# Performance work log

Measured on AMD Instinct MI355X. Metric: run time of the kernel, lower is better.

## Reference

```python
import jax, jax.numpy as jnp
import numpy as np

N_NODES = 50000
N_EDGES = 600000
IN_F = 128
OUT_F = 128
SMALL = max(IN_F // 10, 1)  # floor(128/10) = 12
D_K = np.sqrt(SMALL).astype(np.float32)


def setup_inputs() -> dict:
    key = jax.random.key(0)
    ks = jax.random.split(key, 10)
    node_data = jax.random.normal(ks[0], (N_NODES, IN_F), dtype=jnp.float32)
    src = jax.random.randint(ks[1], (N_EDGES,), 0, N_NODES, dtype=jnp.int32)
    dst = jax.random.randint(ks[2], (N_EDGES,), 0, N_NODES, dtype=jnp.int32)
    s_q = 1.0 / np.sqrt(IN_F)
    Wq = jax.random.uniform(ks[3], (SMALL, IN_F), jnp.float32, -s_q, s_q)
    bq = jax.random.uniform(ks[4], (SMALL,), jnp.float32, -s_q, s_q)
    Wk = jax.random.uniform(ks[5], (SMALL, IN_F), jnp.float32, -s_q, s_q)
    bk = jax.random.uniform(ks[6], (SMALL,), jnp.float32, -s_q, s_q)
    W1 = jax.random.uniform(ks[7], (OUT_F, IN_F), jnp.float32, -s_q, s_q)
    W2 = jax.random.uniform(ks[8], (OUT_F, IN_F), jnp.float32, -s_q, s_q)
    b2 = jax.random.uniform(ks[9], (OUT_F,), jnp.float32, -s_q, s_q)
    return {"node_data": node_data, "src": src, "dst": dst,
            "Wq": Wq, "bq": bq, "Wk": Wk, "bk": bk,
            "W1": W1, "W2": W2, "b2": b2}


def reference(node_data, src, dst, Wq, bq, Wk, bk, W1, W2, b2):
    N = node_data.shape[0]
    # dgl.add_self_loop: append (i, i) for every node -> each dst has >= 1 edge
    loops = jnp.arange(N, dtype=src.dtype)
    s = jnp.concatenate([src, loops])
    d = jnp.concatenate([dst, loops])

    # query = Tanh(Linear), key = Linear  (shapes [N, SMALL])
    q = jnp.tanh(node_data @ Wq.T + bq)
    k = node_data @ Wk.T + bk

    # per-edge score: sum(query[src] * key[dst]) / sqrt(small)
    scores = jnp.sum(q[s] * k[d], axis=1) / D_K  # [E]

    # softmax over incoming edges of each dst node (segment softmax)
    seg_max = jax.ops.segment_max(scores, d, num_segments=N)
    w = jnp.exp(scores - seg_max[d])
    seg_sum = jax.ops.segment_sum(w, d, num_segments=N)
    w = w / seg_sum[d]  # [E]

    # weighted scatter-aggregate of src node inputs -> [N, IN_F]
    att = jax.ops.segment_sum(w[:, None] * node_data[s], d, num_segments=N)

    # DeepSetLayer: layer1(node_data) + layer2(node attention)
    x = node_data @ W1.T + (att @ W2.T + b2)
    # per-row L2 ('fro' over dim=1) normalization, then ReLU
    x = x / jnp.linalg.norm(x, axis=1, keepdims=True)
    return jax.nn.relu(x)
```

## Files before the change

### kernel.cpp

```cpp
#include <hip/hip_runtime.h>
#include <hip/hip_bf16.h>
#include <math.h>
#include <stdint.h>


#define IN_F 128
#define SMALL 12
#define QK_PAD 16
#define SCAN_ITEMS 8
#define SCAN_CHUNK 2048

typedef __attribute__((ext_vector_type(8))) _Float16 half8;
typedef __attribute__((ext_vector_type(8))) unsigned short ushort8;
typedef __attribute__((ext_vector_type(4))) float f32x4;

__device__ __forceinline__ float dot12(const float* __restrict__ qrow,
                                       float4 c0, float4 c1, float4 c2) {
    float4 a = ((const float4*)qrow)[0];
    float4 b = ((const float4*)qrow)[1];
    float4 c = ((const float4*)qrow)[2];
    return a.x*c0.x + a.y*c0.y + a.z*c0.z + a.w*c0.w
         + b.x*c1.x + b.y*c1.y + b.z*c1.z + b.w*c1.w
         + c.x*c2.x + c.y*c2.y + c.z*c2.z + c.w*c2.w;
}

__device__ __forceinline__ half8 ld_h8(const float* p) {
    float4 x0 = *(const float4*)p;
    float4 x1 = *(const float4*)(p + 4);
    half8 a;
    a[0] = (_Float16)x0.x; a[1] = (_Float16)x0.y;
    a[2] = (_Float16)x0.z; a[3] = (_Float16)x0.w;
    a[4] = (_Float16)x1.x; a[5] = (_Float16)x1.y;
    a[6] = (_Float16)x1.z; a[7] = (_Float16)x1.w;
    return a;
}

__global__ __launch_bounds__(256) void prep_kernel(
    const float* __restrict__ nd,
    const float* __restrict__ Wq, const float* __restrict__ bq,
    const float* __restrict__ Wk, const float* __restrict__ bk,
    const int* __restrict__ dst,
    const float* __restrict__ W1, const float* __restrict__ W2,
    float* __restrict__ q, float* __restrict__ kf,
    unsigned short* __restrict__ ndb, int* __restrict__ cnt,
    unsigned short* __restrict__ rank, unsigned short* __restrict__ Wc,
    int N, int E, int NBQK, int NBCNT)
{
    int t = threadIdx.x;
    int b = blockIdx.x;

    if (b < NBQK) {
        int wv = t >> 6;
        int lane = t & 63;
        int col = lane & 15;
        int quad = lane >> 4;
        int tbase = b * 64 + wv * 16;

        int arow = tbase + col;
        int rowc = (arow < N) ? arow : (N - 1);
        const float* ap = nd + (size_t)rowc * IN_F + quad * 8;
        unsigned short* np = ndb + (size_t)arow * IN_F + quad * 8;

        const float* w0 = ((col < 12) ? (Wq + (size_t)col * IN_F)
                                      : (Wk + (size_t)(col - 12) * IN_F)) + quad * 8;
        const float* w1 = Wk + (size_t)((col < 8) ? (col + 4) : 4) * IN_F + quad * 8;
        bool hasw1 = (col < 8);

        half8 zero = {};
        f32x4 acc0 = (f32x4)0.f, acc1 = (f32x4)0.f;
#pragma unroll
        for (int ks = 0; ks < 4; ks++) {
            int k0 = ks * 32;
            half8 a = ld_h8(ap + k0);
            if (arow < N) *(half8*)(np + k0) = a;
            half8 bb0 = ld_h8(w0 + k0);
            half8 bb1 = hasw1 ? ld_h8(w1 + k0) : zero;
            acc0 = __builtin_amdgcn_mfma_f32_16x16x32_f16(a, bb0, acc0, 0, 0, 0);
            acc1 = __builtin_amdgcn_mfma_f32_16x16x32_f16(a, bb1, acc1, 0, 0, 0);
        }
        float bias0 = (col < 12) ? bq[col] : bk[col - 12];
        float bias1 = (col < 8) ? bk[col + 4] : 0.f;
#pragma unroll
        for (int r = 0; r < 4; r++) {
            int node = tbase + quad * 4 + r;
            if (node < N) {
                float v0 = acc0[r] + bias0;
                if (col < 12) q[(size_t)node * QK_PAD + col] = tanhf(v0);
                else          kf[(size_t)node * QK_PAD + (col - 12)] = v0;
                if (hasw1)    kf[(size_t)node * QK_PAD + col + 4] = acc1[r] + bias1;
            }
        }
    } else if (b < NBQK + NBCNT) {
        int ET = E + N;
        int stride = NBCNT * 256;
        for (int i = (b - NBQK) * 256 + t; i < ET; i += stride) {
            int d = (i < E) ? dst[i] : (i - E);
            rank[i] = (unsigned short)atomicAdd(&cnt[d], 1);
        }
    } else {
        int idx = (b - NBQK - NBCNT) * 256 + t;
        int f = idx >> 8, k = idx & 255;
        float v = (k < 128) ? W1[f * 128 + k] : W2[f * 128 + (k - 128)];
        ((_Float16*)Wc)[idx] = (_Float16)v;
    }
}

__global__ __launch_bounds__(256) void scan_local_kernel(
    const int* __restrict__ cnt, int* __restrict__ off,
    int* __restrict__ bsum, int N)
{
    __shared__ int tsum[256];
    int t = threadIdx.x;
    int base = blockIdx.x * SCAN_CHUNK + t * SCAN_ITEMS;
    int v[SCAN_ITEMS];
    int s = 0;
#pragma unroll
    for (int i = 0; i < SCAN_ITEMS; i++) {
        int idx = base + i;
        v[i] = (idx < N) ? ((cnt[idx] + 7) & ~7) : 0;
        s += v[i];
    }
    tsum[t] = s;
    __syncthreads();
    for (int d = 1; d < 256; d <<= 1) {
        int x = (t >= d) ? tsum[t - d] : 0;
        __syncthreads();
        tsum[t] += x;
        __syncthreads();
    }
    int excl = (t == 0) ? 0 : tsum[t - 1];
#pragma unroll
    for (int i = 0; i < SCAN_ITEMS; i++) {
        int idx = base + i;
        if (idx < N) off[idx] = excl;
        excl += v[i];
    }
    if (t == 255) bsum[blockIdx.x] = tsum[255];
}

__global__ __launch_bounds__(256) void scan_add_kernel(
    int* __restrict__ off, const int* __restrict__ bsum, int N, int NB)
{
    __shared__ int pre2[2];
    int t = threadIdx.x;
    if (t == 0) {
        int p = 0, tot = 0;
        for (int i = 0; i < NB; i++) {
            int v = bsum[i];
            if (i < (int)blockIdx.x) p += v;
            tot += v;
        }
        pre2[0] = p; pre2[1] = tot;
    }
    __syncthreads();
    int add = pre2[0];
    if (blockIdx.x == 0 && t == 0) off[N] = pre2[1];

    int base = blockIdx.x * SCAN_CHUNK + t * SCAN_ITEMS;
#pragma unroll
    for (int i = 0; i < SCAN_ITEMS; i++) {
        int j = base + i;
        if (j < N) off[j] += add;
    }
}

__global__ __launch_bounds__(256) void scatter_kernel(
    const int* __restrict__ src, const int* __restrict__ dst,
    const int* __restrict__ off, const unsigned short* __restrict__ rank,
    unsigned short* __restrict__ esrc, int E, int N)
{
    int i = blockIdx.x * 256 + threadIdx.x;
    if (i >= E + N) return;
    int d, s;
    if (i < E) { d = dst[i]; s = src[i]; }
    else       { d = i - E; s = d; }
    esrc[off[d] + (int)rank[i]] = (unsigned short)s;
}

__global__ __launch_bounds__(256) void attn_kernel(
    const unsigned short* __restrict__ ndb, const float* __restrict__ q,
    const float* __restrict__ kf, const int* __restrict__ off,
    const int* __restrict__ cnt, const unsigned short* __restrict__ esrc,
    void* __restrict__ attv, int att16, int N)
{
    const float INVDK = 0.28867513459481287f;
    int t = threadIdx.x;
    int lane = t & 63;
    int l16 = lane & 15;
    int gbase = lane & 48;
    int wid = blockIdx.x * 16 + (t >> 4);
    if (wid >= N) return;

    int start = off[wid];
    int deg = cnt[wid];

    const float4* kp = (const float4*)(kf + (size_t)wid * QK_PAD);
    float4 c0 = kp[0], c1 = kp[1], c2 = kp[2];

    float acc[8];
#pragma unroll
    for (int j = 0; j < 8; j++) acc[j] = 0.f;
    float inv;

    const unsigned short* nb = ndb + l16 * 8;

#define ACCUM(hv, ww) do {                                                    \
        acc[0] += (ww) * (float)(hv)[0]; acc[1] += (ww) * (float)(hv)[1];     \
        acc[2] += (ww) * (float)(hv)[2]; acc[3] += (ww) * (float)(hv)[3];     \
        acc[4] += (ww) * (float)(hv)[4]; acc[5] += (ww) * (float)(hv)[5];     \
        acc[6] += (ww) * (float)(hv)[6]; acc[7] += (ww) * (float)(hv)[7];     \
    } while (0)

#define LOAD8(pfx, id)                                                        \
    half8 pfx##0 = *(const half8*)(nb + (size_t)(id)[0] * IN_F);              \
    half8 pfx##1 = *(const half8*)(nb + (size_t)(id)[1] * IN_F);              \
    half8 pfx##2 = *(const half8*)(nb + (size_t)(id)[2] * IN_F);              \
    half8 pfx##3 = *(const half8*)(nb + (size_t)(id)[3] * IN_F);              \
    half8 pfx##4 = *(const half8*)(nb + (size_t)(id)[4] * IN_F);              \
    half8 pfx##5 = *(const half8*)(nb + (size_t)(id)[5] * IN_F);              \
    half8 pfx##6 = *(const half8*)(nb + (size_t)(id)[6] * IN_F);              \
    half8 pfx##7 = *(const half8*)(nb + (size_t)(id)[7] * IN_F)

#define SHFL8(wsrc, base)                                                     \
    do { _Pragma("unroll")                                                    \
         for (int _i = 0; _i < 8; _i++) wa[_i] = __shfl((wsrc), gbase | ((base) + _i)); } while (0)

#define ACCUM8(pfx) do {                                                      \
        ACCUM(pfx##0, wa[0]); ACCUM(pfx##1, wa[1]);                           \
        ACCUM(pfx##2, wa[2]); ACCUM(pfx##3, wa[3]);                           \
        ACCUM(pfx##4, wa[4]); ACCUM(pfx##5, wa[5]);                           \
        ACCUM(pfx##6, wa[6]); ACCUM(pfx##7, wa[7]); } while (0)

    if (deg <= 32) {
        ushort8 pk0 = *(const ushort8*)(esrc + start);
        ushort8 pk1 = *(const ushort8*)(esrc + start + 8);

        int id0[8];
#pragma unroll
        for (int i = 0; i < 8; i++) id0[i] = (i < deg) ? (int)pk0[i] : 0;
        LOAD8(v, id0);

        int si = (int)esrc[start + l16];
        float sc = -INFINITY;
        if (l16 < deg)
            sc = dot12(q + (size_t)si * QK_PAD, c0, c1, c2) * INVDK;
        float sc1 = -INFINITY;
        if (deg > 16) {
            int si1 = (int)esrc[start + 16 + l16];
            if (16 + l16 < deg)
                sc1 = dot12(q + (size_t)si1 * QK_PAD, c0, c1, c2) * INVDK;
        }
        float m = fmaxf(sc, sc1);
#pragma unroll
        for (int o = 8; o > 0; o >>= 1) m = fmaxf(m, __shfl_xor(m, o));
        float w  = (l16 < deg)      ? __expf(sc - m)  : 0.f;
        float w1 = (16 + l16 < deg) ? __expf(sc1 - m) : 0.f;
        float ls = w + w1;
#pragma unroll
        for (int o = 8; o > 0; o >>= 1) ls += __shfl_xor(ls, o);
        inv = 1.f / ls;

        int id1[8];
#pragma unroll
        for (int i = 0; i < 8; i++) id1[i] = (8 + i < deg) ? (int)pk1[i] : 0;
        LOAD8(u, id1);

        float wa[8];
        SHFL8(w, 0);
        ACCUM8(v);
        SHFL8(w, 8);
        ACCUM8(u);

        if (deg > 16) {
            ushort8 pk2 = *(const ushort8*)(esrc + start + 16);
            ushort8 pk3 = *(const ushort8*)(esrc + start + 24);
            int id2[8], id3[8];
#pragma unroll
            for (int i = 0; i < 8; i++) id2[i] = (16 + i < deg) ? (int)pk2[i] : 0;
#pragma unroll
            for (int i = 0; i < 8; i++) id3[i] = (24 + i < deg) ? (int)pk3[i] : 0;
            LOAD8(x, id2);
            LOAD8(y, id3);
            SHFL8(w1, 0);
            ACCUM8(x);
            SHFL8(w1, 8);
            ACCUM8(y);
        }
    } else {
        float m = -INFINITY;
        for (int i = l16; i < deg; i += 16) {
            int s2 = (int)esrc[start + i];
            m = fmaxf(m, dot12(q + (size_t)s2 * QK_PAD, c0, c1, c2) * INVDK);
        }
#pragma unroll
        for (int o = 8; o > 0; o >>= 1) m = fmaxf(m, __shfl_xor(m, o));
        float ls = 0.f;
        for (int i = l16; i < deg; i += 16) {
            int s2 = (int)esrc[start + i];
            ls += __expf(dot12(q + (size_t)s2 * QK_PAD, c0, c1, c2) * INVDK - m);
        }
#pragma unroll
        for (int o = 8; o > 0; o >>= 1) ls += __shfl_xor(ls, o);
        inv = 1.f / ls;

        for (int base2 = 0; base2 < deg; base2 += 16) {
            int cnt2 = deg - base2; if (cnt2 > 16) cnt2 = 16;
            float w = 0.f; int si = 0;
            if (l16 < cnt2) {
                si = (int)esrc[start + base2 + l16];
                w = __expf(dot12(q + (size_t)si * QK_PAD, c0, c1, c2) * INVDK - m);
            }
            int i = 0;
            for (; i + 4 <= cnt2; i += 4) {
                float u0 = __shfl(w, gbase | i);       int s0 = __shfl(si, gbase | i);
                float u1 = __shfl(w, gbase | (i + 1)); int s1 = __shfl(si, gbase | (i + 1));
                float u2 = __shfl(w, gbase | (i + 2)); int s2 = __shfl(si, gbase | (i + 2));
                float u3 = __shfl(w, gbase | (i + 3)); int s3 = __shfl(si, gbase | (i + 3));
                half8 x0 = *(const half8*)(nb + (size_t)s0 * IN_F);
                half8 x1 = *(const half8*)(nb + (size_t)s1 * IN_F);
                half8 x2 = *(const half8*)(nb + (size_t)s2 * IN_F);
                half8 x3 = *(const half8*)(nb + (size_t)s3 * IN_F);
                ACCUM(x0, u0); ACCUM(x1, u1); ACCUM(x2, u2); ACCUM(x3, u3);
            }
            for (; i < cnt2; i++) {
                float wi = __shfl(w, gbase | i);
                int ri = __shfl(si, gbase | i);
                half8 x = *(const half8*)(nb + (size_t)ri * IN_F);
                ACCUM(x, wi);
            }
        }
    }
#undef ACCUM8
#undef SHFL8
#undef LOAD8
#undef ACCUM

    if (att16) {
        unsigned short* op = (unsigned short*)attv + (size_t)wid * IN_F + l16 * 8;
        half8 st;
#pragma unroll
        for (int j = 0; j < 8; j++) st[j] = (_Float16)(acc[j] * inv);
        *(half8*)op = st;
    } else {
        float* op = (float*)attv + (size_t)wid * IN_F + l16 * 8;
        float4 s0, s1;
        s0.x = acc[0] * inv; s0.y = acc[1] * inv; s0.z = acc[2] * inv; s0.w = acc[3] * inv;
        s1.x = acc[4] * inv; s1.y = acc[5] * inv; s1.z = acc[6] * inv; s1.w = acc[7] * inv;
        *(float4*)op = s0;
        *(float4*)(op + 4) = s1;
    }
}

__global__ __launch_bounds__(256) void final_kernel(
    const unsigned short* __restrict__ ndb, const float* __restrict__ nd,
    const void* __restrict__ attv, int att16,
    const unsigned short* __restrict__ Wc, const float* __restrict__ b2,
    float* __restrict__ out, int N)
{
    int wv = threadIdx.x >> 6;
    int lane = threadIdx.x & 63;
    int col = lane & 15;
    int quad = lane >> 4;

    int arow = blockIdx.x * 64 + wv * 16 + col;
    int rowc = (arow < N) ? arow : (N - 1);
    const unsigned short* a0p = ndb + (size_t)rowc * IN_F + quad * 8;
    const unsigned short* a1h = (const unsigned short*)attv + (size_t)rowc * IN_F + quad * 8;
    const float* a1f = ((arow < N) ? (const float*)attv : nd) + (size_t)rowc * IN_F + quad * 8;

    f32x4 acc[8];
#pragma unroll
    for (int i = 0; i < 8; i++) acc[i] = (f32x4)0.f;

#pragma unroll
    for (int ks = 0; ks < 8; ks++) {
        int k0 = ks * 32;
        half8 a;
        if (ks < 4)      a = *(const half8*)(a0p + k0);
        else if (att16)  a = *(const half8*)(a1h + (k0 - 128));
        else             a = ld_h8(a1f + (k0 - 128));
#pragma unroll
        for (int ft = 0; ft < 8; ft++) {
            int n = ft * 16 + col;
            half8 bb = *(const half8*)(Wc + (size_t)n * 256 + k0 + quad * 8);
            acc[ft] = __builtin_amdgcn_mfma_f32_16x16x32_f16(a, bb, acc[ft], 0, 0, 0);
        }
    }

    float bias[8];
#pragma unroll
    for (int ft = 0; ft < 8; ft++) bias[ft] = b2[ft * 16 + col];

#pragma unroll
    for (int r = 0; r < 4; r++) {
        int node = blockIdx.x * 64 + wv * 16 + quad * 4 + r;
        float v[8];
        float ps = 0.f;
#pragma unroll
        for (int ft = 0; ft < 8; ft++) {
            v[ft] = acc[ft][r] + bias[ft];
            ps += v[ft] * v[ft];
        }
        ps += __shfl_xor(ps, 1);
        ps += __shfl_xor(ps, 2);
        ps += __shfl_xor(ps, 4);
        ps += __shfl_xor(ps, 8);
        float rn = rsqrtf(ps);
        if (node < N) {
            float* op = out + (size_t)node * 128 + col;
#pragma unroll
            for (int ft = 0; ft < 8; ft++)
                op[ft * 16] = fmaxf(v[ft] * rn, 0.f);
        }
    }
}

static inline char* align_up(char* p, size_t a) {
    return (char*)(((uintptr_t)p + (a - 1)) & ~(uintptr_t)(a - 1));
}

extern "C" void kernel_launch(void* const* d_in, const int* in_sizes, int n_in,
                              void* d_out, int out_size, void* d_ws, size_t ws_size,
                              hipStream_t stream) {
    const float* node_data = (const float*)d_in[0];
    const int*   src       = (const int*)d_in[1];
    const int*   dst       = (const int*)d_in[2];
    const float* Wq        = (const float*)d_in[3];
    const float* bq        = (const float*)d_in[4];
    const float* Wk        = (const float*)d_in[5];
    const float* bk        = (const float*)d_in[6];
    const float* W1        = (const float*)d_in[7];
    const float* W2        = (const float*)d_in[8];
    const float* b2        = (const float*)d_in[9];
    float* out = (float*)d_out;

    int N = in_sizes[0] / IN_F;
    int E = in_sizes[1];
    int ET = E + N;
    int EPAD = E + 8 * N + 64;
    int NB = (N + SCAN_CHUNK - 1) / SCAN_CHUNK;
    int NBQK = (N + 63) / 64;
    int NBCNT = 512;
    int NBCVT = 128;

    char* w = (char*)d_ws;
    float* q  = (float*)w;  w += (size_t)N * QK_PAD * sizeof(float);
    float* kf = (float*)w;  w += (size_t)N * QK_PAD * sizeof(float);
    w = align_up(w, 256);
    unsigned short* ndb = (unsigned short*)w;  w += (size_t)N * IN_F * sizeof(unsigned short);
    w = align_up(w, 256);
    unsigned short* Wc = (unsigned short*)w;  w += 128 * 256 * sizeof(unsigned short);
    int* cnt  = (int*)w;  w += (size_t)N * sizeof(int);
    int* off  = (int*)w;  w += (size_t)(N + 1) * sizeof(int);
    int* bsum = (int*)w;  w += 256 * sizeof(int);
    unsigned short* rank = (unsigned short*)w;  w += (size_t)ET * sizeof(unsigned short);
    w = align_up(w, 256);
    unsigned short* esrc = (unsigned short*)w;  w += (size_t)EPAD * sizeof(unsigned short);

    w = align_up(w, 256);
    int att16 = 0;
    void* attp = out;
    if ((size_t)(w - (char*)d_ws) + (size_t)N * IN_F * sizeof(unsigned short) <= ws_size) {
        att16 = 1;
        attp = w;
    }

    hipMemsetAsync(cnt, 0, (size_t)N * sizeof(int), stream);

    prep_kernel<<<NBQK + NBCNT + NBCVT, 256, 0, stream>>>(
        node_data, Wq, bq, Wk, bk, dst, W1, W2,
        q, kf, ndb, cnt, rank, Wc, N, E, NBQK, NBCNT);
    scan_local_kernel<<<NB, 256, 0, stream>>>(cnt, off, bsum, N);
    scan_add_kernel<<<NB, 256, 0, stream>>>(off, bsum, N, NB);
    scatter_kernel<<<(ET + 255) / 256, 256, 0, stream>>>(src, dst, off, rank, esrc, E, N);
    attn_kernel<<<(N + 15) / 16, 256, 0, stream>>>(ndb, q, kf, off, cnt, esrc, attp, att16, N);
    final_kernel<<<(N + 63) / 64, 256, 0, stream>>>(ndb, node_data, attp, att16, Wc, b2, out, N);
}
```

Baseline: 207.5 us.

## Fuse attention aggregation with final MFMA projection through shared memory

Merges the attention gather kernel and the final linear/normalize kernel into one kernel. Each block processes 64 nodes in four 16-node passes, prefetching the next pass's offsets, key vectors and edge indices, and writes the fp16 attention rows to LDS instead of global memory. The MFMA stage then reads the attention half from LDS, removing the global write and re-read of the intermediate and one kernel launch. In exchange it uses fewer, heavier blocks (4x fewer attention threads launched) with added LDS, which may lower the parallelism available to hide gather latency.

```diff
diff --git a/kernel.cpp b/kernel.cpp
--- a/kernel.cpp
+++ b/kernel.cpp
@@ -177,32 +177,32 @@
     esrc[off[d] + (int)rank[i]] = (unsigned short)s;
 }
 
-__global__ __launch_bounds__(256) void attn_kernel(
+__global__ __launch_bounds__(256) void attn_final_kernel(
     const unsigned short* __restrict__ ndb, const float* __restrict__ q,
     const float* __restrict__ kf, const int* __restrict__ off,
     const int* __restrict__ cnt, const unsigned short* __restrict__ esrc,
-    void* __restrict__ attv, int att16, int N)
+    const unsigned short* __restrict__ Wc, const float* __restrict__ b2,
+    float* __restrict__ out, int N)
 {
+    __shared__ _Float16 satt[64][136];
     const float INVDK = 0.28867513459481287f;
     int t = threadIdx.x;
-    int lane = t & 63;
-    int l16 = lane & 15;
-    int gbase = lane & 48;
-    int wid = blockIdx.x * 16 + (t >> 4);
-    if (wid >= N) return;
-
-    int start = off[wid];
-    int deg = cnt[wid];
-
-    const float4* kp = (const float4*)(kf + (size_t)wid * QK_PAD);
-    float4 c0 = kp[0], c1 = kp[1], c2 = kp[2];
-
-    float acc[8];
-#pragma unroll
-    for (int j = 0; j < 8; j++) acc[j] = 0.f;
-    float inv;
+    int grp = t >> 4;
+    int l16 = t & 15;
+    int gbase = (t & 63) & 48;
+    int nbase = blockIdx.x * 64;
 
     const unsigned short* nb = ndb + l16 * 8;
+
+    int st, dg; float4 c0, c1, c2; ushort8 p0, p1;
+    {
+        int w0i = nbase + grp; if (w0i >= N) w0i = N - 1;
+        st = off[w0i]; dg = cnt[w0i];
+        const float4* kp = (const float4*)(kf + (size_t)w0i * QK_PAD);
+        c0 = kp[0]; c1 = kp[1]; c2 = kp[2];
+        p0 = *(const ushort8*)(esrc + st);
+        p1 = *(const ushort8*)(esrc + st + 8);
+    }
 
 #define ACCUM(hv, ww) do {                                                    \
         acc[0] += (ww) * (float)(hv)[0]; acc[1] += (ww) * (float)(hv)[1];     \
@@ -231,159 +231,160 @@
         ACCUM(pfx##4, wa[4]); ACCUM(pfx##5, wa[5]);                           \
         ACCUM(pfx##6, wa[6]); ACCUM(pfx##7, wa[7]); } while (0)
 
-    if (deg <= 32) {
-        ushort8 pk0 = *(const ushort8*)(esrc + start);
-        ushort8 pk1 = *(const ushort8*)(esrc + start + 8);
-
-        int id0[8];
-#pragma unroll
-        for (int i = 0; i < 8; i++) id0[i] = (i < deg) ? (int)pk0[i] : 0;
-        LOAD8(v, id0);
-
-        int si = (int)esrc[start + l16];
-        float sc = -INFINITY;
-        if (l16 < deg)
-            sc = dot12(q + (size_t)si * QK_PAD, c0, c1, c2) * INVDK;
-        float sc1 = -INFINITY;
-        if (deg > 16) {
-            int si1 = (int)esrc[start + 16 + l16];
-            if (16 + l16 < deg)
-                sc1 = dot12(q + (size_t)si1 * QK_PAD, c0, c1, c2) * INVDK;
-        }
-        float m = fmaxf(sc, sc1);
-#pragma unroll
-        for (int o = 8; o > 0; o >>= 1) m = fmaxf(m, __shfl_xor(m, o));
-        float w  = (l16 < deg)      ? __expf(sc - m)  : 0.f;
-        float w1 = (16 + l16 < deg) ? __expf(sc1 - m) : 0.f;
-        float ls = w + w1;
-#pragma unroll
-        for (int o = 8; o > 0; o >>= 1) ls += __shfl_xor(ls, o);
-        inv = 1.f / ls;
-
-        int id1[8];
-#pragma unroll
-        for (int i = 0; i < 8; i++) id1[i] = (8 + i < deg) ? (int)pk1[i] : 0;
-        LOAD8(u, id1);
-
-        float wa[8];
-        SHFL8(w, 0);
-        ACCUM8(v);
-        SHFL8(w, 8);
-        ACCUM8(u);
-
-        if (deg > 16) {
-            ushort8 pk2 = *(const ushort8*)(esrc + start + 16);
-            ushort8 pk3 = *(const ushort8*)(esrc + start + 24);
-            int id2[8], id3[8];
-#pragma unroll
-            for (int i = 0; i < 8; i++) id2[i] = (16 + i < deg) ? (int)pk2[i] : 0;
-#pragma unroll
-            for (int i = 0; i < 8; i++) id3[i] = (24 + i < deg) ? (int)pk3[i] : 0;
-            LOAD8(x, id2);
-            LOAD8(y, id3);
-            SHFL8(w1, 0);
-            ACCUM8(x);
-            SHFL8(w1, 8);
-            ACCUM8(y);
-        }
-    } else {
-        float m = -INFINITY;
-        for (int i = l16; i < deg; i += 16) {
-            int s2 = (int)esrc[start + i];
-            m = fmaxf(m, dot12(q + (size_t)s2 * QK_PAD, c0, c1, c2) * INVDK);
-        }
-#pragma unroll
-        for (int o = 8; o > 0; o >>= 1) m = fmaxf(m, __shfl_xor(m, o));
-        float ls = 0.f;
-        for (int i = l16; i < deg; i += 16) {
-            int s2 = (int)esrc[start + i];
-            ls += __expf(dot12(q + (size_t)s2 * QK_PAD, c0, c1, c2) * INVDK - m);
-        }
-#pragma unroll
-        for (int o = 8; o > 0; o >>= 1) ls += __shfl_xor(ls, o);
-        inv = 1.f / ls;
-
-        for (int base2 = 0; base2 < deg; base2 += 16) {
-            int cnt2 = deg - base2; if (cnt2 > 16) cnt2 = 16;
-            float w = 0.f; int si = 0;
-            if (l16 < cnt2) {
-                si = (int)esrc[start + base2 + l16];
-                w = __expf(dot12(q + (size_t)si * QK_PAD, c0, c1, c2) * INVDK - m);
-            }
-            int i = 0;
-            for (; i + 4 <= cnt2; i += 4) {
-                float u0 = __shfl(w, gbase | i);       int s0 = __shfl(si, gbase | i);
-                float u1 = __shfl(w, gbase | (i + 1)); int s1 = __shfl(si, gbase | (i + 1));
-                float u2 = __shfl(w, gbase | (i + 2)); int s2 = __shfl(si, gbase | (i + 2));
-                float u3 = __shfl(w, gbase | (i + 3)); int s3 = __shfl(si, gbase | (i + 3));
-                half8 x0 = *(const half8*)(nb + (size_t)s0 * IN_F);
-                half8 x1 = *(const half8*)(nb + (size_t)s1 * IN_F);
-                half8 x2 = *(const half8*)(nb + (size_t)s2 * IN_F);
-                half8 x3 = *(const half8*)(nb + (size_t)s3 * IN_F);
-                ACCUM(x0, u0); ACCUM(x1, u1); ACCUM(x2, u2); ACCUM(x3, u3);
-            }
-            for (; i < cnt2; i++) {
-                float wi = __shfl(w, gbase | i);
-                int ri = __shfl(si, gbase | i);
-                half8 x = *(const half8*)(nb + (size_t)ri * IN_F);
-                ACCUM(x, wi);
-            }
-        }
+    for (int it = 0; it < 4; ++it) {
+        float acc[8];
+#pragma unroll
+        for (int j = 0; j < 8; j++) acc[j] = 0.f;
+        float inv;
+
+        int stN = 0, dgN = 0; float4 c0N = c0, c1N = c1, c2N = c2;
+        ushort8 p0N = p0, p1N = p1;
+        if (it < 3) {
+            int wn = nbase + (it + 1) * 16 + grp; if (wn >= N) wn = N - 1;
+            stN = off[wn]; dgN = cnt[wn];
+            const float4* kp = (const float4*)(kf + (size_t)wn * QK_PAD);
+            c0N = kp[0]; c1N = kp[1]; c2N = kp[2];
+            p0N = *(const ushort8*)(esrc + stN);
+            p1N = *(const ushort8*)(esrc + stN + 8);
+        }
+
+        if (dg <= 32) {
+            int id0[8];
+#pragma unroll
+            for (int i = 0; i < 8; i++) id0[i] = (i < dg) ? (int)p0[i] : 0;
+            LOAD8(v, id0);
+
+            int si = (int)esrc[st + l16];
+            float sc = -INFINITY;
+            if (l16 < dg)
+                sc = dot12(q + (size_t)si * QK_PAD, c0, c1, c2) * INVDK;
+            float sc1 = -INFINITY;
+            if (dg > 16) {
+                int si1 = (int)esrc[st + 16 + l16];
+                if (16 + l16 < dg)
+                    sc1 = dot12(q + (size_t)si1 * QK_PAD, c0, c1, c2) * INVDK;
+            }
+            float m = fmaxf(sc, sc1);
+#pragma unroll
+            for (int o = 8; o > 0; o >>= 1) m = fmaxf(m, __shfl_xor(m, o));
+            float w  = (l16 < dg)      ? __expf(sc - m)  : 0.f;
+            float w1 = (16 + l16 < dg) ? __expf(sc1 - m) : 0.f;
+            float ls = w + w1;
+#pragma unroll
+            for (int o = 8; o > 0; o >>= 1) ls += __shfl_xor(ls, o);
+            inv = 1.f / ls;
+
+            int id1[8];
+#pragma unroll
+            for (int i = 0; i < 8; i++) id1[i] = (8 + i < dg) ? (int)p1[i] : 0;
+            LOAD8(u, id1);
+
+            float wa[8];
+            SHFL8(w, 0);
+            ACCUM8(v);
+            SHFL8(w, 8);
+            ACCUM8(u);
+
+            if (dg > 16) {
+                ushort8 pk2 = *(const ushort8*)(esrc + st + 16);
+                ushort8 pk3 = *(const ushort8*)(esrc + st + 24);
+                int id2[8], id3[8];
+#pragma unroll
+                for (int i = 0; i < 8; i++) id2[i] = (16 + i < dg) ? (int)pk2[i] : 0;
+#pragma unroll
+                for (int i = 0; i < 8; i++) id3[i] = (24 + i < dg) ? (int)pk3[i] : 0;
+                LOAD8(x, id2);
+                LOAD8(y, id3);
+                SHFL8(w1, 0);
+                ACCUM8(x);
+                SHFL8(w1, 8);
+                ACCUM8(y);
+            }
+        } else {
+            float m = -INFINITY;
+            for (int i = l16; i < dg; i += 16) {
+                int s2 = (int)esrc[st + i];
+                m = fmaxf(m, dot12(q + (size_t)s2 * QK_PAD, c0, c1, c2) * INVDK);
+            }
+#pragma unroll
+            for (int o = 8; o > 0; o >>= 1) m = fmaxf(m, __shfl_xor(m, o));
+            float ls = 0.f;
+            for (int i = l16; i < dg; i += 16) {
+                int s2 = (int)esrc[st + i];
+                ls += __expf(dot12(q + (size_t)s2 * QK_PAD, c0, c1, c2) * INVDK - m);
+            }
+#pragma unroll
+            for (int o = 8; o > 0; o >>= 1) ls += __shfl_xor(ls, o);
+            inv = 1.f / ls;
+
+            for (int base2 = 0; base2 < dg; base2 += 16) {
+                int cnt2 = dg - base2; if (cnt2 > 16) cnt2 = 16;
+                float w = 0.f; int si = 0;
+                if (l16 < cnt2) {
+                    si = (int)esrc[st + base2 + l16];
+                    w = __expf(dot12(q + (size_t)si * QK_PAD, c0, c1, c2) * INVDK - m);
+                }
+                int i = 0;
+                for (; i + 4 <= cnt2; i += 4) {
+                    float u0 = __shfl(w, gbase | i);       int s0 = __shfl(si, gbase | i);
+                    float u1 = __shfl(w, gbase | (i + 1)); int s1 = __shfl(si, gbase | (i + 1));
+                    float u2 = __shfl(w, gbase | (i + 2)); int s2 = __shfl(si, gbase | (i + 2));
+                    float u3 = __shfl(w, gbase | (i + 3)); int s3 = __shfl(si, gbase | (i + 3));
+                    half8 x0 = *(const half8*)(nb + (size_t)s0 * IN_F);
+                    half8 x1 = *(const half8*)(nb + (size_t)s1 * IN_F);
+                    half8 x2 = *(const half8*)(nb + (size_t)s2 * IN_F);
+                    half8 x3 = *(const half8*)(nb + (size_t)s3 * IN_F);
+                    ACCUM(x0, u0); ACCUM(x1, u1); ACCUM(x2, u2); ACCUM(x3, u3);
+                }
+                for (; i < cnt2; i++) {
+                    float wi = __shfl(w, gbase | i);
+                    int ri = __shfl(si, gbase | i);
+                    half8 x = *(const half8*)(nb + (size_t)ri * IN_F);
+                    ACCUM(x, wi);
+                }
+            }
+        }
+
+        {
+            half8 stv;
+#pragma unroll
+            for (int j = 0; j < 8; j++) stv[j] = (_Float16)(acc[j] * inv);
+            *(half8*)&satt[it * 16 + grp][l16 * 8] = stv;
+        }
+
+        st = stN; dg = dgN; c0 = c0N; c1 = c1N; c2 = c2N; p0 = p0N; p1 = p1N;
     }
 #undef ACCUM8
 #undef SHFL8
 #undef LOAD8
 #undef ACCUM
 
-    if (att16) {
-        unsigned short* op = (unsigned short*)attv + (size_t)wid * IN_F + l16 * 8;
-        half8 st;
-#pragma unroll
-        for (int j = 0; j < 8; j++) st[j] = (_Float16)(acc[j] * inv);
-        *(half8*)op = st;
-    } else {
-        float* op = (float*)attv + (size_t)wid * IN_F + l16 * 8;
-        float4 s0, s1;
-        s0.x = acc[0] * inv; s0.y = acc[1] * inv; s0.z = acc[2] * inv; s0.w = acc[3] * inv;
-        s1.x = acc[4] * inv; s1.y = acc[5] * inv; s1.z = acc[6] * inv; s1.w = acc[7] * inv;
-        *(float4*)op = s0;
-        *(float4*)(op + 4) = s1;
-    }
-}
-
-__global__ __launch_bounds__(256) void final_kernel(
-    const unsigned short* __restrict__ ndb, const float* __restrict__ nd,
-    const void* __restrict__ attv, int att16,
-    const unsigned short* __restrict__ Wc, const float* __restrict__ b2,
-    float* __restrict__ out, int N)
-{
-    int wv = threadIdx.x >> 6;
-    int lane = threadIdx.x & 63;
+    __syncthreads();
+
+    int wv = t >> 6;
+    int lane = t & 63;
     int col = lane & 15;
     int quad = lane >> 4;
 
-    int arow = blockIdx.x * 64 + wv * 16 + col;
+    int arow = nbase + wv * 16 + col;
     int rowc = (arow < N) ? arow : (N - 1);
     const unsigned short* a0p = ndb + (size_t)rowc * IN_F + quad * 8;
-    const unsigned short* a1h = (const unsigned short*)attv + (size_t)rowc * IN_F + quad * 8;
-    const float* a1f = ((arow < N) ? (const float*)attv : nd) + (size_t)rowc * IN_F + quad * 8;
-
-    f32x4 acc[8];
-#pragma unroll
-    for (int i = 0; i < 8; i++) acc[i] = (f32x4)0.f;
+
+    f32x4 facc[8];
+#pragma unroll
+    for (int i = 0; i < 8; i++) facc[i] = (f32x4)0.f;
 
 #pragma unroll
     for (int ks = 0; ks < 8; ks++) {
         int k0 = ks * 32;
         half8 a;
-        if (ks < 4)      a = *(const half8*)(a0p + k0);
-        else if (att16)  a = *(const half8*)(a1h + (k0 - 128));
-        else             a = ld_h8(a1f + (k0 - 128));
+        if (ks < 4) a = *(const half8*)(a0p + k0);
+        else        a = *(const half8*)&satt[wv * 16 + col][(ks - 4) * 32 + quad * 8];
 #pragma unroll
         for (int ft = 0; ft < 8; ft++) {
             int n = ft * 16 + col;
             half8 bb = *(const half8*)(Wc + (size_t)n * 256 + k0 + quad * 8);
-            acc[ft] = __builtin_amdgcn_mfma_f32_16x16x32_f16(a, bb, acc[ft], 0, 0, 0);
+            facc[ft] = __builtin_amdgcn_mfma_f32_16x16x32_f16(a, bb, facc[ft], 0, 0, 0);
         }
     }
 
@@ -393,12 +394,12 @@
 
 #pragma unroll
     for (int r = 0; r < 4; r++) {
-        int node = blockIdx.x * 64 + wv * 16 + quad * 4 + r;
+        int node = nbase + wv * 16 + quad * 4 + r;
         float v[8];
         float ps = 0.f;
 #pragma unroll
         for (int ft = 0; ft < 8; ft++) {
-            v[ft] = acc[ft][r] + bias[ft];
+            v[ft] = facc[ft][r] + bias[ft];
             ps += v[ft] * v[ft];
         }
         ps += __shfl_xor(ps, 1);
@@ -457,14 +458,6 @@
     w = align_up(w, 256);
     unsigned short* esrc = (unsigned short*)w;  w += (size_t)EPAD * sizeof(unsigned short);
 
-    w = align_up(w, 256);
-    int att16 = 0;
-    void* attp = out;
-    if ((size_t)(w - (char*)d_ws) + (size_t)N * IN_F * sizeof(unsigned short) <= ws_size) {
-        att16 = 1;
-        attp = w;
-    }
-
     hipMemsetAsync(cnt, 0, (size_t)N * sizeof(int), stream);
 
     prep_kernel<<<NBQK + NBCNT + NBCVT, 256, 0, stream>>>(
@@ -473,6 +466,6 @@
     scan_local_kernel<<<NB, 256, 0, stream>>>(cnt, off, bsum, N);
     scan_add_kernel<<<NB, 256, 0, stream>>>(off, bsum, N, NB);
     scatter_kernel<<<(ET + 255) / 256, 256, 0, stream>>>(src, dst, off, rank, esrc, E, N);
-    attn_kernel<<<(N + 15) / 16, 256, 0, stream>>>(ndb, q, kf, off, cnt, esrc, attp, att16, N);
-    final_kernel<<<(N + 63) / 64, 256, 0, stream>>>(ndb, node_data, attp, att16, Wc, b2, out, N);
-}
+    attn_final_kernel<<<(N + 63) / 64, 256, 0, stream>>>(
+        ndb, q, kf, off, cnt, esrc, Wc, b2, out, N);
+}
```

Measured after the change: 213.1 us. +2.7%, slower.
